# Kernel optimization log

Measured on AMD Instinct MI355X. Metric: run time of the kernel, lower is better.

Reference implementation:

```python
import jax, jax.numpy as jnp
import numpy as np

B, S, D = 64, 512, 1024  # batch, seq_len, units (input_dim == units required by module)
UNITS = D


def setup_inputs() -> dict:
    key = jax.random.key(0)
    k1, k2, k3 = jax.random.split(key, 3)
    inputs = jax.random.normal(k1, (B, S, D), dtype=jnp.float32)
    # kernel / recurrent_kernel: (input_dim, 4*units), gate column order [i, f, c, o]
    scale = 1.0 / np.sqrt(D)
    W = jax.random.normal(k2, (D, 4 * UNITS), dtype=jnp.float32) * scale
    U = jax.random.normal(k3, (D, 4 * UNITS), dtype=jnp.float32) * scale
    b = jnp.zeros((4 * UNITS,), dtype=jnp.float32)
    return {"inputs": inputs, "W": W, "U": U, "b": b}


def _lstm(inputs, W, U, b):
    units = W.shape[1] // 4
    h0 = jnp.zeros((inputs.shape[0], units), dtype=inputs.dtype)
    c0 = jnp.zeros((inputs.shape[0], units), dtype=inputs.dtype)
    # Precompute input projections for all timesteps in one big GEMM: [B,S,4U]
    x_proj = jnp.einsum("bsd,dg->bsg", inputs, W) + b
    x_proj_t = jnp.swapaxes(x_proj, 0, 1)  # [S,B,4U] time-major

    def step(carry, xp):
        ht, ct = carry
        z = xp + ht @ U  # [B,4U]
        i = jax.nn.sigmoid(z[:, :units])
        f = jax.nn.sigmoid(z[:, units:2 * units])
        c_t = jnp.tanh(z[:, 2 * units:3 * units])
        o = jax.nn.sigmoid(z[:, 3 * units:])
        ct = f * ct + i * c_t
        ht = o * jnp.tanh(ct)
        return (ht, ct), ht

    (ht, ct), outs = jax.lax.scan(step, (h0, c0), x_proj_t)
    outputs = jnp.swapaxes(outs, 0, 1)  # [B,S,U]
    return outputs, ht, ct


def reference(inputs, W, U, b):
    return _lstm(inputs, W, U, b)
```

## Files before the change

### kernel.cpp

```cpp
#include <hip/hip_runtime.h>
#include <hip/hip_bf16.h>
#include <cstdint>
#include <cstddef>

#define BB 64
#define SS 512
#define DD 1024
#define G4 4096

typedef __attribute__((ext_vector_type(8))) short bf16x8;
typedef __attribute__((ext_vector_type(8))) unsigned short u16x8;
typedef __attribute__((ext_vector_type(4))) float f32x4;

static __device__ __forceinline__ unsigned short f2bf(float f) {
  union { float f; uint32_t u; } v; v.f = f;
  uint32_t u = v.u;
  return (unsigned short)((u + 0x7FFFu + ((u >> 16) & 1u)) >> 16);
}
static __device__ __forceinline__ float bf2f(unsigned short s) {
  union { uint32_t u; float f; } v; v.u = ((uint32_t)s) << 16; return v.f;
}

typedef __attribute__((address_space(1))) const unsigned int kGlbU32;
typedef __attribute__((address_space(3))) unsigned int kLdsU32;
static __device__ __forceinline__ void gload_lds16(const void* g, void* l) {
  __builtin_amdgcn_global_load_lds((kGlbU32*)g, (kLdsU32*)l, 16, 0, 0);
}

__global__ void cvt_x(const float* __restrict__ in, unsigned short* __restrict__ out, int n8) {
  for (int i = blockIdx.x * blockDim.x + threadIdx.x; i < n8; i += gridDim.x * blockDim.x) {
    const float4* pp = (const float4*)(in + (size_t)i * 8);
    float4 a = pp[0], b2 = pp[1];
    u16x8 o;
    o[0] = f2bf(a.x);  o[1] = f2bf(a.y);  o[2] = f2bf(a.z);  o[3] = f2bf(a.w);
    o[4] = f2bf(b2.x); o[5] = f2bf(b2.y); o[6] = f2bf(b2.z); o[7] = f2bf(b2.w);
    *(u16x8*)(out + (size_t)i * 8) = o;
  }
}

__global__ __launch_bounds__(256) void cvt_transpose(
    const float* __restrict__ Win, const float* __restrict__ Uin,
    unsigned short* __restrict__ Wt, unsigned short* __restrict__ Ut) {
  __shared__ float tile[32][33];
  const float* in = blockIdx.z ? Uin : Win;
  unsigned short* out = blockIdx.z ? Ut : Wt;
  int k0 = blockIdx.x * 32;
  int c0 = blockIdx.y * 32;
  int tc = threadIdx.x & 31, tr = threadIdx.x >> 5;
  #pragma unroll
  for (int j = 0; j < 32; j += 8)
    tile[tr + j][tc] = in[(size_t)(k0 + tr + j) * G4 + (c0 + tc)];
  __syncthreads();
  #pragma unroll
  for (int j = 0; j < 32; j += 8)
    out[(size_t)(c0 + tr + j) * DD + (k0 + tc)] = f2bf(tile[tc][tr + j]);
}

__global__ __launch_bounds__(256) void pack_u(const unsigned short* __restrict__ Ut,
                                              unsigned short* __restrict__ Up) {
  int tid = blockIdx.x * 256 + threadIdx.x;
  int l = tid & 63;
  int kk = (tid >> 6) & 31;
  int g = (tid >> 11) & 3;
  int u = tid >> 13;
  int col = g * DD + u * 16 + (l & 15);
  int k = kk * 32 + (l >> 4) * 8;
  bf16x8 v = *(const bf16x8*)(Ut + (size_t)col * DD + k);
  *(bf16x8*)(Up + (size_t)tid * 8) = v;
}

__global__ __launch_bounds__(256) void gemm_xproj(
    const unsigned short* __restrict__ xb,
    const unsigned short* __restrict__ Wt,
    const float* __restrict__ bias,
    unsigned short* __restrict__ xproj) {
  __shared__ unsigned short As[128 * 64], Bs[128 * 64];
  const int tid = threadIdx.x;
  const int wave = tid >> 6, lane = tid & 63;
  const int wr = wave >> 1, wc = wave & 1;
  const int m0 = blockIdx.x * 128, n0 = blockIdx.y * 128;

  const int srow = tid >> 1, shalf = tid & 1;
  const unsigned short* ga = xb + (size_t)(m0 + srow) * DD + shalf * 32;
  const unsigned short* gb = Wt + (size_t)(n0 + srow) * DD + shalf * 32;

  bf16x8 ra[4], rb[4];
  #pragma unroll
  for (int c = 0; c < 4; ++c) {
    ra[c] = *(const bf16x8*)(ga + c * 8);
    rb[c] = *(const bf16x8*)(gb + c * 8);
  }

  f32x4 acc[4][4];
  #pragma unroll
  for (int m = 0; m < 4; ++m)
    #pragma unroll
    for (int n = 0; n < 4; ++n) acc[m][n] = (f32x4){0.f, 0.f, 0.f, 0.f};

  char* asb = (char*)As;
  char* bsb = (char*)Bs;

  for (int kt = 0; kt < DD / 64; ++kt) {
    __syncthreads();
    #pragma unroll
    for (int c = 0; c < 4; ++c) {
      int wb = srow * 128 + ((shalf * 64 + c * 16) ^ ((srow & 7) << 4));
      *(bf16x8*)(asb + wb) = ra[c];
      *(bf16x8*)(bsb + wb) = rb[c];
    }
    __syncthreads();
    if (kt + 1 < DD / 64) {
      #pragma unroll
      for (int c = 0; c < 4; ++c) {
        ra[c] = *(const bf16x8*)(ga + (kt + 1) * 64 + c * 8);
        rb[c] = *(const bf16x8*)(gb + (kt + 1) * 64 + c * 8);
      }
    }
    #pragma unroll
    for (int kh = 0; kh < 2; ++kh) {
      bf16x8 af[4], bfr[4];
      const int kb = kh * 64 + (lane >> 4) * 16;
      #pragma unroll
      for (int m = 0; m < 4; ++m) {
        int row = wr * 64 + m * 16 + (lane & 15);
        af[m] = *(const bf16x8*)(asb + row * 128 + (kb ^ ((row & 7) << 4)));
        int coln = wc * 64 + m * 16 + (lane & 15);
        bfr[m] = *(const bf16x8*)(bsb + coln * 128 + (kb ^ ((coln & 7) << 4)));
      }
      #pragma unroll
      for (int m = 0; m < 4; ++m)
        #pragma unroll
        for (int n = 0; n < 4; ++n)
          acc[m][n] = __builtin_amdgcn_mfma_f32_16x16x32_bf16(af[m], bfr[n], acc[m][n], 0, 0, 0);
    }
  }

  #pragma unroll
  for (int n = 0; n < 4; ++n) {
    int col = n0 + wc * 64 + n * 16 + (lane & 15);
    int g = col >> 10, unit = col & 1023;
    int ugrp2 = unit >> 4, uc2 = unit & 15;
    float bv = bias[col];
    #pragma unroll
    for (int m = 0; m < 4; ++m) {
      #pragma unroll
      for (int j = 0; j < 4; ++j) {
        int mrow = m0 + wr * 64 + m * 16 + (lane >> 4) * 4 + j;
        int b = mrow >> 9, t2 = mrow & 511;
        size_t idx = ((((size_t)t2 * 4 + (b >> 4)) * 64 + ugrp2) * 256 + (b & 15) * 16 + uc2) * 4 + g;
        xproj[idx] = f2bf(acc[m][n][j] + bv);
      }
    }
  }
}

__global__ __launch_bounds__(256, 1) void lstm_persist(
    const unsigned short* __restrict__ xproj,
    const unsigned short* __restrict__ Up,
    unsigned short* __restrict__ h0,
    unsigned short* __restrict__ h1,
    unsigned int* __restrict__ bar,
    float* __restrict__ out) {
  extern __shared__ char smem[];
  const int bid = blockIdx.x;
  const int rgrp = (bid & 7) >> 1;
  const int ugrp = (bid >> 3) * 2 + (bid & 1);
  const int tid = threadIdx.x;
  const int wave = tid >> 6, lane = tid & 63;
  const int r = tid >> 4, uc = tid & 15;
  const int row = rgrp * 16 + r, unit = ugrp * 16 + uc;

  char* upw = smem + wave * 30720;
  float (*zt)[16][16] = (float (*)[16][16])(smem + 122880);

  const char* ug = (const char*)Up + (size_t)(ugrp * 4 + wave) * 32768;
  #pragma unroll
  for (int kk = 0; kk < 30; ++kk)
    gload_lds16(ug + kk * 1024 + lane * 16, upw + kk * 1024 + lane * 16);
  bf16x8 u30 = *(const bf16x8*)(ug + 30 * 1024 + lane * 16);
  bf16x8 u31 = *(const bf16x8*)(ug + 31 * 1024 + lane * 16);

  const unsigned short* xp = xproj + (((size_t)rgrp * 64 + ugrp) * 256 + tid) * 4;
  const int hnidx = ((rgrp * 32 + (unit >> 5)) * 64 + ((unit >> 3) & 3) * 16 + r) * 8 + (unit & 7);
  unsigned int* myflags = bar + rgrp * 64;
  float c = 0.f;
  ushort4 xv = *(const ushort4*)xp;

  asm volatile("s_waitcnt vmcnt(0)" ::: "memory");
  __builtin_amdgcn_sched_barrier(0);
  __syncthreads();

  const bf16x8* uv = (const bf16x8*)upw;
  f32x4 z4 = {0.f, 0.f, 0.f, 0.f};
  unsigned fv = 0;

  for (int t = 0; t < SS; ++t) {
    #pragma unroll
    for (int j = 0; j < 4; ++j)
      zt[wave][(lane >> 4) * 4 + j][lane & 15] = z4[j];
    __syncthreads();

    float zi = zt[0][r][uc] + bf2f(xv.x);
    float zf = zt[1][r][uc] + bf2f(xv.y);
    float zg = zt[2][r][uc] + bf2f(xv.z);
    float zo = zt[3][r][uc] + bf2f(xv.w);
    float ig = 1.f / (1.f + __expf(-zi));
    float fg = 1.f / (1.f + __expf(-zf));
    float gg = 1.f - 2.f / (1.f + __expf(2.f * zg));
    float og = 1.f / (1.f + __expf(-zo));
    c = fg * c + ig * gg;
    float h = og * (1.f - 2.f / (1.f + __expf(2.f * c)));

    if (t == SS - 1) {
      out[((size_t)row * SS + t) * DD + unit] = h;
      const size_t S0 = (size_t)BB * SS * DD;
      out[S0 + (size_t)row * DD + unit] = h;
      out[S0 + (size_t)BB * DD + (size_t)row * DD + unit] = c;
      break;
    }

    unsigned short* hn = (t & 1) ? h0 : h1;
    __hip_atomic_store(hn + hnidx, f2bf(h), __ATOMIC_RELAXED, __HIP_MEMORY_SCOPE_AGENT);
    __syncthreads();
    if (tid == 0)
      __hip_atomic_store(myflags + ugrp, (unsigned)(t + 1), __ATOMIC_RELAXED, __HIP_MEMORY_SCOPE_AGENT);
    out[((size_t)row * SS + t) * DD + unit] = h;
    xv = *(const ushort4*)(xp + (size_t)(t + 1) * 262144);

    const char* hb = (const char*)((t & 1) ? h0 : h1) + rgrp * 32768 + lane * 16;
    const unsigned tgt = (unsigned)(t + 1);
    f32x4 a0 = {0.f,0.f,0.f,0.f}, a1 = a0, a2 = a0, a3 = a0;
    #pragma unroll
    for (int b = 0; b < 4; ++b) {
      while ((( __ballot((int)(fv >= tgt)) >> (16 * b)) & 0xFFFFull) != 0xFFFFull)
        fv = __hip_atomic_load(myflags + lane, __ATOMIC_RELAXED, __HIP_MEMORY_SCOPE_AGENT);
      bf16x8 av0, av1, av2, av3, av4, av5, av6, av7;
      const char* hbb = hb + b * 8192;
      asm volatile("global_load_dwordx4 %0, %1, off sc0 sc1" : "=v"(av0) : "v"(hbb + 0 * 1024) : "memory");
      asm volatile("global_load_dwordx4 %0, %1, off sc0 sc1" : "=v"(av1) : "v"(hbb + 1 * 1024) : "memory");
      asm volatile("global_load_dwordx4 %0, %1, off sc0 sc1" : "=v"(av2) : "v"(hbb + 2 * 1024) : "memory");
      asm volatile("global_load_dwordx4 %0, %1, off sc0 sc1" : "=v"(av3) : "v"(hbb + 3 * 1024) : "memory");
      asm volatile("global_load_dwordx4 %0, %1, off sc0 sc1" : "=v"(av4) : "v"(hbb + 4 * 1024) : "memory");
      asm volatile("global_load_dwordx4 %0, %1, off sc0 sc1" : "=v"(av5) : "v"(hbb + 5 * 1024) : "memory");
      asm volatile("global_load_dwordx4 %0, %1, off sc0 sc1" : "=v"(av6) : "v"(hbb + 6 * 1024) : "memory");
      asm volatile("global_load_dwordx4 %0, %1, off sc0 sc1" : "=v"(av7) : "v"(hbb + 7 * 1024) : "memory");
      asm volatile("s_waitcnt vmcnt(0)" ::: "memory");
      __builtin_amdgcn_sched_barrier(0);
      const int k0 = b * 8;
      a0 = __builtin_amdgcn_mfma_f32_16x16x32_bf16(av0, (k0 + 0 < 30) ? uv[(k0 + 0) * 64 + lane] : ((k0 + 0 == 30) ? u30 : u31), a0, 0, 0, 0);
      a1 = __builtin_amdgcn_mfma_f32_16x16x32_bf16(av1, (k0 + 1 < 30) ? uv[(k0 + 1) * 64 + lane] : ((k0 + 1 == 30) ? u30 : u31), a1, 0, 0, 0);
      a2 = __builtin_amdgcn_mfma_f32_16x16x32_bf16(av2, (k0 + 2 < 30) ? uv[(k0 + 2) * 64 + lane] : ((k0 + 2 == 30) ? u30 : u31), a2, 0, 0, 0);
      a3 = __builtin_amdgcn_mfma_f32_16x16x32_bf16(av3, (k0 + 3 < 30) ? uv[(k0 + 3) * 64 + lane] : ((k0 + 3 == 30) ? u30 : u31), a3, 0, 0, 0);
      a0 = __builtin_amdgcn_mfma_f32_16x16x32_bf16(av4, (k0 + 4 < 30) ? uv[(k0 + 4) * 64 + lane] : ((k0 + 4 == 30) ? u30 : u31), a0, 0, 0, 0);
      a1 = __builtin_amdgcn_mfma_f32_16x16x32_bf16(av5, (k0 + 5 < 30) ? uv[(k0 + 5) * 64 + lane] : ((k0 + 5 == 30) ? u30 : u31), a1, 0, 0, 0);
      a2 = __builtin_amdgcn_mfma_f32_16x16x32_bf16(av6, (k0 + 6 < 30) ? uv[(k0 + 6) * 64 + lane] : ((k0 + 6 == 30) ? u30 : u31), a2, 0, 0, 0);
      a3 = __builtin_amdgcn_mfma_f32_16x16x32_bf16(av7, (k0 + 7 < 30) ? uv[(k0 + 7) * 64 + lane] : ((k0 + 7 == 30) ? u30 : u31), a3, 0, 0, 0);
    }
    z4 = (a0 + a1) + (a2 + a3);
  }
}

template <bool XBF>
__global__ __launch_bounds__(256) void lstm_step(
    const unsigned short* __restrict__ xb, const float* __restrict__ xf,
    const unsigned short* __restrict__ Wt, const unsigned short* __restrict__ Ut,
    const float* __restrict__ bias, unsigned short* __restrict__ hbuf,
    float* __restrict__ cbuf, float* __restrict__ out, int t) {
  __shared__ float ztl[4][16][16];
  const int wg = blockIdx.x;
  const int ugrp = wg >> 2, rgrp = wg & 3;
  const int row0 = rgrp * 16;
  const int ucol0 = ugrp * 16;
  const int wave = threadIdx.x >> 6;
  const int lane = threadIdx.x & 63;
  const int k0 = (lane >> 4) * 8;
  const int gr = row0 + (lane & 15);
  const int cg = wave * DD + ucol0 + (lane & 15);

  const unsigned short* hp = hbuf + (size_t)(t & 1) * BB * DD + (size_t)gr * DD + k0;
  const unsigned short* wp = Wt + (size_t)cg * DD + k0;
  const unsigned short* up = Ut + (size_t)cg * DD + k0;

  f32x4 acc = {0.f, 0.f, 0.f, 0.f};
  if (XBF) {
    const unsigned short* xpp = xb + ((size_t)gr * SS + t) * DD + k0;
    #pragma unroll 8
    for (int kk = 0; kk < DD; kk += 32) {
      bf16x8 a = *(const bf16x8*)(xpp + kk);
      bf16x8 b = *(const bf16x8*)(wp + kk);
      acc = __builtin_amdgcn_mfma_f32_16x16x32_bf16(a, b, acc, 0, 0, 0);
    }
  } else {
    const float* xpp = xf + ((size_t)gr * SS + t) * DD + k0;
    #pragma unroll 4
    for (int kk = 0; kk < DD; kk += 32) {
      float4 v0 = *(const float4*)(xpp + kk);
      float4 v1 = *(const float4*)(xpp + kk + 4);
      bf16x8 a;
      a[0] = (short)f2bf(v0.x); a[1] = (short)f2bf(v0.y);
      a[2] = (short)f2bf(v0.z); a[3] = (short)f2bf(v0.w);
      a[4] = (short)f2bf(v1.x); a[5] = (short)f2bf(v1.y);
      a[6] = (short)f2bf(v1.z); a[7] = (short)f2bf(v1.w);
      bf16x8 b = *(const bf16x8*)(wp + kk);
      acc = __builtin_amdgcn_mfma_f32_16x16x32_bf16(a, b, acc, 0, 0, 0);
    }
  }
  #pragma unroll 8
  for (int kk = 0; kk < DD; kk += 32) {
    bf16x8 a = *(const bf16x8*)(hp + kk);
    bf16x8 b = *(const bf16x8*)(up + kk);
    acc = __builtin_amdgcn_mfma_f32_16x16x32_bf16(a, b, acc, 0, 0, 0);
  }

  float bv = bias[cg];
  #pragma unroll
  for (int j = 0; j < 4; ++j)
    ztl[wave][(lane >> 4) * 4 + j][lane & 15] = acc[j] + bv;
  __syncthreads();

  const int r = threadIdx.x >> 4, uc = threadIdx.x & 15;
  float zi = ztl[0][r][uc], zf = ztl[1][r][uc], zg = ztl[2][r][uc], zo = ztl[3][r][uc];
  float ig = 1.f / (1.f + __expf(-zi));
  float fg = 1.f / (1.f + __expf(-zf));
  float gg = tanhf(zg);
  float og = 1.f / (1.f + __expf(-zo));
  const int gidx = (row0 + r) * DD + ucol0 + uc;
  float c = fg * cbuf[gidx] + ig * gg;
  cbuf[gidx] = c;
  float h = og * tanhf(c);
  hbuf[(size_t)((t & 1) ^ 1) * BB * DD + gidx] = f2bf(h);
  out[((size_t)(row0 + r) * SS + t) * DD + ucol0 + uc] = h;
  if (t == SS - 1) {
    out[(size_t)BB * SS * DD + gidx] = h;
    out[(size_t)BB * SS * DD + BB * DD + gidx] = c;
  }
}

extern "C" void kernel_launch(void* const* d_in, const int* in_sizes, int n_in,
                              void* d_out, int out_size, void* d_ws, size_t ws_size,
                              hipStream_t stream) {
  const float* x = (const float*)d_in[0];
  const float* W = (const float*)d_in[1];
  const float* U = (const float*)d_in[2];
  const float* bias = (const float*)d_in[3];
  float* out = (float*)d_out;
  char* ws = (char*)d_ws;

  const size_t oWt = 0;
  const size_t oUt = oWt + (size_t)G4 * DD * 2;
  const size_t oH0 = oUt + (size_t)G4 * DD * 2;
  const size_t oH1 = oH0 + (size_t)BB * DD * 2;
  const size_t oC  = oH1 + (size_t)BB * DD * 2;
  const size_t oBar = oC + (size_t)BB * DD * 4;
  const size_t oXb = oBar + 4096;
  const size_t oUp = oXb + (size_t)BB * SS * DD * 2;
  const size_t oXp = oUp + (size_t)G4 * DD * 2;
  const size_t needPersist = oXp + (size_t)SS * BB * G4 * 2;
  const size_t needR1x = oUp;

  unsigned short* Wt = (unsigned short*)(ws + oWt);
  unsigned short* Ut = (unsigned short*)(ws + oUt);
  unsigned short* h0 = (unsigned short*)(ws + oH0);
  unsigned short* h1 = (unsigned short*)(ws + oH1);
  float* cbuf = (float*)(ws + oC);
  unsigned int* bar = (unsigned int*)(ws + oBar);
  unsigned short* xb = (unsigned short*)(ws + oXb);
  unsigned short* Up = (unsigned short*)(ws + oUp);
  unsigned short* xproj = (unsigned short*)(ws + oXp);

  if (ws_size >= needPersist) {
    hipFuncSetAttribute((const void*)lstm_persist,
                        hipFuncAttributeMaxDynamicSharedMemorySize, 126976);
    hipMemsetAsync(h0, 0, (size_t)BB * DD * 2, stream);
    hipMemsetAsync(bar, 0, 4096, stream);
    cvt_transpose<<<dim3(32, 128, 2), 256, 0, stream>>>(W, U, Wt, Ut);
    pack_u<<<2048, 256, 0, stream>>>(Ut, Up);
    cvt_x<<<2048, 256, 0, stream>>>(x, xb, BB * SS * DD / 8);
    gemm_xproj<<<dim3(256, 32), 256, 0, stream>>>(xb, Wt, bias, xproj);
    lstm_persist<<<256, 256, 126976, stream>>>(xproj, Up, h0, h1, bar, out);
  } else {
    unsigned short* hbuf = h0;
    const bool xbf = ws_size >= needR1x;
    hipMemsetAsync(hbuf, 0, (size_t)2 * BB * DD * 2 + (size_t)BB * DD * 4, stream);
    cvt_transpose<<<dim3(32, 128, 2), 256, 0, stream>>>(W, U, Wt, Ut);
    if (xbf) cvt_x<<<2048, 256, 0, stream>>>(x, xb, BB * SS * DD / 8);
    for (int t = 0; t < SS; ++t) {
      if (xbf)
        lstm_step<true><<<256, 256, 0, stream>>>(xb, nullptr, Wt, Ut, bias, hbuf, cbuf, out, t);
      else
        lstm_step<false><<<256, 256, 0, stream>>>(nullptr, x, Wt, Ut, bias, hbuf, cbuf, out, t);
    }
  }
}
```

Before: 2.462 ms.

## Wait on all flags once, then load full hidden state via atomic loads

Replaces the staged per-quarter flag polling plus inline-asm sc0/sc1 loads with one wait on all 64 producer flags, followed by 64 relaxed 64-bit atomic loads of the whole hidden vector. It also remaps the thread-to-(row,unit) assignment so each thread's h store goes to a contiguous offset (hoff = ... + tid). The intent is to drop the repeated ballot/poll rounds and issue all h loads back to back before the MFMA chain. In exchange, loading can no longer overlap with producers that finish late, register pressure rises from 64 live 64-bit values, and coherence now depends on atomic-load semantics instead of explicit cache-bypass flags.

```diff
diff --git a/kernel.cpp b/kernel.cpp
--- a/kernel.cpp
+++ b/kernel.cpp
@@ -167,8 +167,10 @@
   const int ugrp = (bid >> 3) * 2 + (bid & 1);
   const int tid = threadIdx.x;
   const int wave = tid >> 6, lane = tid & 63;
-  const int r = tid >> 4, uc = tid & 15;
-  const int row = rgrp * 16 + r, unit = ugrp * 16 + uc;
+  const int row = (tid >> 3) & 15;
+  const int uc = (tid >> 7) * 8 + (tid & 7);
+  const int unit = ugrp * 16 + uc;
+  const int grow = rgrp * 16 + row;
 
   char* upw = smem + wave * 30720;
   float (*zt)[16][16] = (float (*)[16][16])(smem + 122880);
@@ -180,8 +182,8 @@
   bf16x8 u30 = *(const bf16x8*)(ug + 30 * 1024 + lane * 16);
   bf16x8 u31 = *(const bf16x8*)(ug + 31 * 1024 + lane * 16);
 
-  const unsigned short* xp = xproj + (((size_t)rgrp * 64 + ugrp) * 256 + tid) * 4;
-  const int hnidx = ((rgrp * 32 + (unit >> 5)) * 64 + ((unit >> 3) & 3) * 16 + r) * 8 + (unit & 7);
+  const unsigned short* xp = xproj + (((size_t)rgrp * 64 + ugrp) * 256 + row * 16 + uc) * 4;
+  const size_t hoff = (size_t)rgrp * 16384 + (size_t)(ugrp >> 1) * 512 + (size_t)(ugrp & 1) * 256 + tid;
   unsigned int* myflags = bar + rgrp * 64;
   float c = 0.f;
   ushort4 xv = *(const ushort4*)xp;
@@ -200,10 +202,10 @@
       zt[wave][(lane >> 4) * 4 + j][lane & 15] = z4[j];
     __syncthreads();
 
-    float zi = zt[0][r][uc] + bf2f(xv.x);
-    float zf = zt[1][r][uc] + bf2f(xv.y);
-    float zg = zt[2][r][uc] + bf2f(xv.z);
-    float zo = zt[3][r][uc] + bf2f(xv.w);
+    float zi = zt[0][row][uc] + bf2f(xv.x);
+    float zf = zt[1][row][uc] + bf2f(xv.y);
+    float zg = zt[2][row][uc] + bf2f(xv.z);
+    float zo = zt[3][row][uc] + bf2f(xv.w);
     float ig = 1.f / (1.f + __expf(-zi));
     float fg = 1.f / (1.f + __expf(-zf));
     float gg = 1.f - 2.f / (1.f + __expf(2.f * zg));
@@ -212,49 +214,50 @@
     float h = og * (1.f - 2.f / (1.f + __expf(2.f * c)));
 
     if (t == SS - 1) {
-      out[((size_t)row * SS + t) * DD + unit] = h;
+      out[((size_t)grow * SS + t) * DD + unit] = h;
       const size_t S0 = (size_t)BB * SS * DD;
-      out[S0 + (size_t)row * DD + unit] = h;
-      out[S0 + (size_t)BB * DD + (size_t)row * DD + unit] = c;
+      out[S0 + (size_t)grow * DD + unit] = h;
+      out[S0 + (size_t)BB * DD + (size_t)grow * DD + unit] = c;
       break;
     }
 
     unsigned short* hn = (t & 1) ? h0 : h1;
-    __hip_atomic_store(hn + hnidx, f2bf(h), __ATOMIC_RELAXED, __HIP_MEMORY_SCOPE_AGENT);
+    __hip_atomic_store(hn + hoff, f2bf(h), __ATOMIC_RELAXED, __HIP_MEMORY_SCOPE_AGENT);
     __syncthreads();
     if (tid == 0)
       __hip_atomic_store(myflags + ugrp, (unsigned)(t + 1), __ATOMIC_RELAXED, __HIP_MEMORY_SCOPE_AGENT);
-    out[((size_t)row * SS + t) * DD + unit] = h;
+    out[((size_t)grow * SS + t) * DD + unit] = h;
     xv = *(const ushort4*)(xp + (size_t)(t + 1) * 262144);
 
-    const char* hb = (const char*)((t & 1) ? h0 : h1) + rgrp * 32768 + lane * 16;
     const unsigned tgt = (unsigned)(t + 1);
+    while (!__all((int)(fv >= tgt)))
+      fv = __hip_atomic_load(myflags + lane, __ATOMIC_RELAXED, __HIP_MEMORY_SCOPE_AGENT);
+
+    const unsigned long long* hq =
+        (const unsigned long long*)((t & 1) ? h0 : h1) + (size_t)rgrp * 4096 + lane * 2;
+    unsigned long long lo[32], hi[32];
+    #pragma unroll
+    for (int i = 0; i < 32; ++i) {
+      lo[i] = __hip_atomic_load(hq + (size_t)i * 128,     __ATOMIC_RELAXED, __HIP_MEMORY_SCOPE_AGENT);
+      hi[i] = __hip_atomic_load(hq + (size_t)i * 128 + 1, __ATOMIC_RELAXED, __HIP_MEMORY_SCOPE_AGENT);
+    }
+
     f32x4 a0 = {0.f,0.f,0.f,0.f}, a1 = a0, a2 = a0, a3 = a0;
     #pragma unroll
-    for (int b = 0; b < 4; ++b) {
-      while ((( __ballot((int)(fv >= tgt)) >> (16 * b)) & 0xFFFFull) != 0xFFFFull)
-        fv = __hip_atomic_load(myflags + lane, __ATOMIC_RELAXED, __HIP_MEMORY_SCOPE_AGENT);
-      bf16x8 av0, av1, av2, av3, av4, av5, av6, av7;
-      const char* hbb = hb + b * 8192;
-      asm volatile("global_load_dwordx4 %0, %1, off sc0 sc1" : "=v"(av0) : "v"(hbb + 0 * 1024) : "memory");
-      asm volatile("global_load_dwordx4 %0, %1, off sc0 sc1" : "=v"(av1) : "v"(hbb + 1 * 1024) : "memory");
-      asm volatile("global_load_dwordx4 %0, %1, off sc0 sc1" : "=v"(av2) : "v"(hbb + 2 * 1024) : "memory");
-      asm volatile("global_load_dwordx4 %0, %1, off sc0 sc1" : "=v"(av3) : "v"(hbb + 3 * 1024) : "memory");
-      asm volatile("global_load_dwordx4 %0, %1, off sc0 sc1" : "=v"(av4) : "v"(hbb + 4 * 1024) : "memory");
-      asm volatile("global_load_dwordx4 %0, %1, off sc0 sc1" : "=v"(av5) : "v"(hbb + 5 * 1024) : "memory");
-      asm volatile("global_load_dwordx4 %0, %1, off sc0 sc1" : "=v"(av6) : "v"(hbb + 6 * 1024) : "memory");
-      asm volatile("global_load_dwordx4 %0, %1, off sc0 sc1" : "=v"(av7) : "v"(hbb + 7 * 1024) : "memory");
-      asm volatile("s_waitcnt vmcnt(0)" ::: "memory");
-      __builtin_amdgcn_sched_barrier(0);
-      const int k0 = b * 8;
-      a0 = __builtin_amdgcn_mfma_f32_16x16x32_bf16(av0, (k0 + 0 < 30) ? uv[(k0 + 0) * 64 + lane] : ((k0 + 0 == 30) ? u30 : u31), a0, 0, 0, 0);
-      a1 = __builtin_amdgcn_mfma_f32_16x16x32_bf16(av1, (k0 + 1 < 30) ? uv[(k0 + 1) * 64 + lane] : ((k0 + 1 == 30) ? u30 : u31), a1, 0, 0, 0);
-      a2 = __builtin_amdgcn_mfma_f32_16x16x32_bf16(av2, (k0 + 2 < 30) ? uv[(k0 + 2) * 64 + lane] : ((k0 + 2 == 30) ? u30 : u31), a2, 0, 0, 0);
-      a3 = __builtin_amdgcn_mfma_f32_16x16x32_bf16(av3, (k0 + 3 < 30) ? uv[(k0 + 3) * 64 + lane] : ((k0 + 3 == 30) ? u30 : u31), a3, 0, 0, 0);
-      a0 = __builtin_amdgcn_mfma_f32_16x16x32_bf16(av4, (k0 + 4 < 30) ? uv[(k0 + 4) * 64 + lane] : ((k0 + 4 == 30) ? u30 : u31), a0, 0, 0, 0);
-      a1 = __builtin_amdgcn_mfma_f32_16x16x32_bf16(av5, (k0 + 5 < 30) ? uv[(k0 + 5) * 64 + lane] : ((k0 + 5 == 30) ? u30 : u31), a1, 0, 0, 0);
-      a2 = __builtin_amdgcn_mfma_f32_16x16x32_bf16(av6, (k0 + 6 < 30) ? uv[(k0 + 6) * 64 + lane] : ((k0 + 6 == 30) ? u30 : u31), a2, 0, 0, 0);
-      a3 = __builtin_amdgcn_mfma_f32_16x16x32_bf16(av7, (k0 + 7 < 30) ? uv[(k0 + 7) * 64 + lane] : ((k0 + 7 == 30) ? u30 : u31), a3, 0, 0, 0);
+    for (int i = 0; i < 32; i += 4) {
+      union { unsigned long long q[2]; bf16x8 v; } w0, w1, w2, w3;
+      w0.q[0] = lo[i + 0]; w0.q[1] = hi[i + 0];
+      w1.q[0] = lo[i + 1]; w1.q[1] = hi[i + 1];
+      w2.q[0] = lo[i + 2]; w2.q[1] = hi[i + 2];
+      w3.q[0] = lo[i + 3]; w3.q[1] = hi[i + 3];
+      bf16x8 b0 = (i + 0 < 30) ? uv[(i + 0) * 64 + lane] : ((i + 0 == 30) ? u30 : u31);
+      bf16x8 b1 = (i + 1 < 30) ? uv[(i + 1) * 64 + lane] : ((i + 1 == 30) ? u30 : u31);
+      bf16x8 b2 = (i + 2 < 30) ? uv[(i + 2) * 64 + lane] : ((i + 2 == 30) ? u30 : u31);
+      bf16x8 b3 = (i + 3 < 30) ? uv[(i + 3) * 64 + lane] : ((i + 3 == 30) ? u30 : u31);
+      a0 = __builtin_amdgcn_mfma_f32_16x16x32_bf16(w0.v, b0, a0, 0, 0, 0);
+      a1 = __builtin_amdgcn_mfma_f32_16x16x32_bf16(w1.v, b1, a1, 0, 0, 0);
+      a2 = __builtin_amdgcn_mfma_f32_16x16x32_bf16(w2.v, b2, a2, 0, 0, 0);
+      a3 = __builtin_amdgcn_mfma_f32_16x16x32_bf16(w3.v, b3, a3, 0, 0, 0);
     }
     z4 = (a0 + a1) + (a2 + a3);
   }
```

New measurement: 2.667 ms. +8.3%, slower.

## Fuse input projection GEMM into persistent LSTM kernel per timestep

Applied to the files above, without the earlier changes.

Removes the separate x·W GEMM and its large bf16 xproj buffer. Each timestep, the persistent kernel now stages the next x rows into LDS and computes its x·W slice with MFMA, reading packed W from global/L2, while other blocks finish the hidden state. This is meant to save the big GEMM pass and the xproj write and read, and to hide the projection work under the barrier wait. In exchange it adds W reads and MFMA work on every step of the serial critical path, and needs more LDS.

```diff
diff --git a/kernel.cpp b/kernel.cpp
--- a/kernel.cpp
+++ b/kernel.cpp
@@ -69,97 +69,14 @@
   *(bf16x8*)(Up + (size_t)tid * 8) = v;
 }
 
-__global__ __launch_bounds__(256) void gemm_xproj(
+__global__ __launch_bounds__(256, 1) void lstm_persist(
     const unsigned short* __restrict__ xb,
-    const unsigned short* __restrict__ Wt,
-    const float* __restrict__ bias,
-    unsigned short* __restrict__ xproj) {
-  __shared__ unsigned short As[128 * 64], Bs[128 * 64];
-  const int tid = threadIdx.x;
-  const int wave = tid >> 6, lane = tid & 63;
-  const int wr = wave >> 1, wc = wave & 1;
-  const int m0 = blockIdx.x * 128, n0 = blockIdx.y * 128;
-
-  const int srow = tid >> 1, shalf = tid & 1;
-  const unsigned short* ga = xb + (size_t)(m0 + srow) * DD + shalf * 32;
-  const unsigned short* gb = Wt + (size_t)(n0 + srow) * DD + shalf * 32;
-
-  bf16x8 ra[4], rb[4];
-  #pragma unroll
-  for (int c = 0; c < 4; ++c) {
-    ra[c] = *(const bf16x8*)(ga + c * 8);
-    rb[c] = *(const bf16x8*)(gb + c * 8);
-  }
-
-  f32x4 acc[4][4];
-  #pragma unroll
-  for (int m = 0; m < 4; ++m)
-    #pragma unroll
-    for (int n = 0; n < 4; ++n) acc[m][n] = (f32x4){0.f, 0.f, 0.f, 0.f};
-
-  char* asb = (char*)As;
-  char* bsb = (char*)Bs;
-
-  for (int kt = 0; kt < DD / 64; ++kt) {
-    __syncthreads();
-    #pragma unroll
-    for (int c = 0; c < 4; ++c) {
-      int wb = srow * 128 + ((shalf * 64 + c * 16) ^ ((srow & 7) << 4));
-      *(bf16x8*)(asb + wb) = ra[c];
-      *(bf16x8*)(bsb + wb) = rb[c];
-    }
-    __syncthreads();
-    if (kt + 1 < DD / 64) {
-      #pragma unroll
-      for (int c = 0; c < 4; ++c) {
-        ra[c] = *(const bf16x8*)(ga + (kt + 1) * 64 + c * 8);
-        rb[c] = *(const bf16x8*)(gb + (kt + 1) * 64 + c * 8);
-      }
-    }
-    #pragma unroll
-    for (int kh = 0; kh < 2; ++kh) {
-      bf16x8 af[4], bfr[4];
-      const int kb = kh * 64 + (lane >> 4) * 16;
-      #pragma unroll
-      for (int m = 0; m < 4; ++m) {
-        int row = wr * 64 + m * 16 + (lane & 15);
-        af[m] = *(const bf16x8*)(asb + row * 128 + (kb ^ ((row & 7) << 4)));
-        int coln = wc * 64 + m * 16 + (lane & 15);
-        bfr[m] = *(const bf16x8*)(bsb + coln * 128 + (kb ^ ((coln & 7) << 4)));
-      }
-      #pragma unroll
-      for (int m = 0; m < 4; ++m)
-        #pragma unroll
-        for (int n = 0; n < 4; ++n)
-          acc[m][n] = __builtin_amdgcn_mfma_f32_16x16x32_bf16(af[m], bfr[n], acc[m][n], 0, 0, 0);
-    }
-  }
-
-  #pragma unroll
-  for (int n = 0; n < 4; ++n) {
-    int col = n0 + wc * 64 + n * 16 + (lane & 15);
-    int g = col >> 10, unit = col & 1023;
-    int ugrp2 = unit >> 4, uc2 = unit & 15;
-    float bv = bias[col];
-    #pragma unroll
-    for (int m = 0; m < 4; ++m) {
-      #pragma unroll
-      for (int j = 0; j < 4; ++j) {
-        int mrow = m0 + wr * 64 + m * 16 + (lane >> 4) * 4 + j;
-        int b = mrow >> 9, t2 = mrow & 511;
-        size_t idx = ((((size_t)t2 * 4 + (b >> 4)) * 64 + ugrp2) * 256 + (b & 15) * 16 + uc2) * 4 + g;
-        xproj[idx] = f2bf(acc[m][n][j] + bv);
-      }
-    }
-  }
-}
-
-__global__ __launch_bounds__(256, 1) void lstm_persist(
-    const unsigned short* __restrict__ xproj,
     const unsigned short* __restrict__ Up,
+    const unsigned short* __restrict__ Wp,
     unsigned short* __restrict__ h0,
     unsigned short* __restrict__ h1,
     unsigned int* __restrict__ bar,
+    const float* __restrict__ bias,
     float* __restrict__ out) {
   extern __shared__ char smem[];
   const int bid = blockIdx.x;
@@ -167,11 +84,14 @@
   const int ugrp = (bid >> 3) * 2 + (bid & 1);
   const int tid = threadIdx.x;
   const int wave = tid >> 6, lane = tid & 63;
-  const int r = tid >> 4, uc = tid & 15;
-  const int row = rgrp * 16 + r, unit = ugrp * 16 + uc;
+  const int row = (tid >> 3) & 15;
+  const int uc = (tid >> 7) * 8 + (tid & 7);
+  const int unit = ugrp * 16 + uc;
+  const int grow = rgrp * 16 + row;
 
   char* upw = smem + wave * 30720;
-  float (*zt)[16][16] = (float (*)[16][16])(smem + 122880);
+  char* xs  = smem + 122880;
+  float (*zt)[16][16] = (float (*)[16][16])(smem + 155648);
 
   const char* ug = (const char*)Up + (size_t)(ugrp * 4 + wave) * 32768;
   #pragma unroll
@@ -179,31 +99,77 @@
     gload_lds16(ug + kk * 1024 + lane * 16, upw + kk * 1024 + lane * 16);
   bf16x8 u30 = *(const bf16x8*)(ug + 30 * 1024 + lane * 16);
   bf16x8 u31 = *(const bf16x8*)(ug + 31 * 1024 + lane * 16);
-
-  const unsigned short* xp = xproj + (((size_t)rgrp * 64 + ugrp) * 256 + tid) * 4;
-  const int hnidx = ((rgrp * 32 + (unit >> 5)) * 64 + ((unit >> 3) & 3) * 16 + r) * 8 + (unit & 7);
+  const char* wgb = (const char*)Wp + (size_t)(ugrp * 4 + wave) * 32768;
+
+  const float bi0 = bias[unit], bi1 = bias[DD + unit],
+              bi2 = bias[2 * DD + unit], bi3 = bias[3 * DD + unit];
+
+  const size_t hoff = (size_t)rgrp * 16384 + (size_t)(ugrp >> 1) * 512 +
+                      (size_t)(ugrp & 1) * 256 + tid;
   unsigned int* myflags = bar + rgrp * 64;
   float c = 0.f;
-  ushort4 xv = *(const ushort4*)xp;
-
+
+#define STAGE_X(TT)                                                            \
+  {                                                                            \
+    _Pragma("unroll")                                                          \
+    for (int i = 0; i < 8; ++i) {                                              \
+      const int ch = wave * 8 + i;                                             \
+      const int xrow = ch >> 1;                                                \
+      const int kbyte = (ch & 1) * 1024 + lane * 16;                           \
+      const int ksw = kbyte ^ ((xrow & 7) << 4);                               \
+      const char* src = (const char*)xb +                                      \
+          ((size_t)(rgrp * 16 + xrow) * SS + (TT)) * 2048 + ksw;               \
+      gload_lds16(src, xs + ch * 1024 + lane * 16);                            \
+    }                                                                          \
+  }
+
+#define XW_COMPUTE(ZXOUT)                                                      \
+  {                                                                            \
+    f32x4 x0 = {0.f, 0.f, 0.f, 0.f}, x1 = x0, x2 = x0, x3 = x0;                \
+    _Pragma("unroll")                                                          \
+    for (int half = 0; half < 2; ++half) {                                     \
+      bf16x8 wv[16];                                                           \
+      _Pragma("unroll")                                                        \
+      for (int i = 0; i < 16; ++i)                                             \
+        wv[i] = *(const bf16x8*)(wgb + (half * 16 + i) * 1024 + lane * 16);    \
+      _Pragma("unroll")                                                        \
+      for (int i = 0; i < 16; i += 4) {                                        \
+        const int kk = half * 16 + i;                                          \
+        const int arow = (lane & 15) * 2048;                                   \
+        const int swz = (lane & 7) << 4;                                       \
+        bf16x8 af0 = *(const bf16x8*)(xs + arow + (((kk + 0) * 64 + (lane >> 4) * 16) ^ swz)); \
+        bf16x8 af1 = *(const bf16x8*)(xs + arow + (((kk + 1) * 64 + (lane >> 4) * 16) ^ swz)); \
+        bf16x8 af2 = *(const bf16x8*)(xs + arow + (((kk + 2) * 64 + (lane >> 4) * 16) ^ swz)); \
+        bf16x8 af3 = *(const bf16x8*)(xs + arow + (((kk + 3) * 64 + (lane >> 4) * 16) ^ swz)); \
+        x0 = __builtin_amdgcn_mfma_f32_16x16x32_bf16(af0, wv[i + 0], x0, 0, 0, 0); \
+        x1 = __builtin_amdgcn_mfma_f32_16x16x32_bf16(af1, wv[i + 1], x1, 0, 0, 0); \
+        x2 = __builtin_amdgcn_mfma_f32_16x16x32_bf16(af2, wv[i + 2], x2, 0, 0, 0); \
+        x3 = __builtin_amdgcn_mfma_f32_16x16x32_bf16(af3, wv[i + 3], x3, 0, 0, 0); \
+      }                                                                        \
+    }                                                                          \
+    ZXOUT = (x0 + x1) + (x2 + x3);                                             \
+  }
+
+  STAGE_X(0);
   asm volatile("s_waitcnt vmcnt(0)" ::: "memory");
   __builtin_amdgcn_sched_barrier(0);
   __syncthreads();
 
-  const bf16x8* uv = (const bf16x8*)upw;
+  f32x4 zx4;
+  XW_COMPUTE(zx4);
   f32x4 z4 = {0.f, 0.f, 0.f, 0.f};
   unsigned fv = 0;
 
   for (int t = 0; t < SS; ++t) {
     #pragma unroll
     for (int j = 0; j < 4; ++j)
-      zt[wave][(lane >> 4) * 4 + j][lane & 15] = z4[j];
+      zt[wave][(lane >> 4) * 4 + j][lane & 15] = z4[j] + zx4[j];
     __syncthreads();
 
-    float zi = zt[0][r][uc] + bf2f(xv.x);
-    float zf = zt[1][r][uc] + bf2f(xv.y);
-    float zg = zt[2][r][uc] + bf2f(xv.z);
-    float zo = zt[3][r][uc] + bf2f(xv.w);
+    float zi = zt[0][row][uc] + bi0;
+    float zf = zt[1][row][uc] + bi1;
+    float zg = zt[2][row][uc] + bi2;
+    float zo = zt[3][row][uc] + bi3;
     float ig = 1.f / (1.f + __expf(-zi));
     float fg = 1.f / (1.f + __expf(-zf));
     float gg = 1.f - 2.f / (1.f + __expf(2.f * zg));
@@ -212,27 +178,33 @@
     float h = og * (1.f - 2.f / (1.f + __expf(2.f * c)));
 
     if (t == SS - 1) {
-      out[((size_t)row * SS + t) * DD + unit] = h;
+      out[((size_t)grow * SS + t) * DD + unit] = h;
       const size_t S0 = (size_t)BB * SS * DD;
-      out[S0 + (size_t)row * DD + unit] = h;
-      out[S0 + (size_t)BB * DD + (size_t)row * DD + unit] = c;
+      out[S0 + (size_t)grow * DD + unit] = h;
+      out[S0 + (size_t)BB * DD + (size_t)grow * DD + unit] = c;
       break;
     }
 
+    STAGE_X(t + 1);
+
     unsigned short* hn = (t & 1) ? h0 : h1;
-    __hip_atomic_store(hn + hnidx, f2bf(h), __ATOMIC_RELAXED, __HIP_MEMORY_SCOPE_AGENT);
+    __hip_atomic_store(hn + hoff, f2bf(h), __ATOMIC_RELAXED, __HIP_MEMORY_SCOPE_AGENT);
     __syncthreads();
     if (tid == 0)
       __hip_atomic_store(myflags + ugrp, (unsigned)(t + 1), __ATOMIC_RELAXED, __HIP_MEMORY_SCOPE_AGENT);
-    out[((size_t)row * SS + t) * DD + unit] = h;
-    xv = *(const ushort4*)(xp + (size_t)(t + 1) * 262144);
-
-    const char* hb = (const char*)((t & 1) ? h0 : h1) + rgrp * 32768 + lane * 16;
+    out[((size_t)grow * SS + t) * DD + unit] = h;
+    XW_COMPUTE(zx4);
+
+    asm volatile("s_waitcnt vmcnt(0)" ::: "memory");
+    __builtin_amdgcn_sched_barrier(0);
+
     const unsigned tgt = (unsigned)(t + 1);
+    const char* hb = (const char*)((t & 1) ? h0 : h1) + (size_t)rgrp * 32768 + lane * 16;
+    const bf16x8* uv = (const bf16x8*)upw;
     f32x4 a0 = {0.f,0.f,0.f,0.f}, a1 = a0, a2 = a0, a3 = a0;
     #pragma unroll
     for (int b = 0; b < 4; ++b) {
-      while ((( __ballot((int)(fv >= tgt)) >> (16 * b)) & 0xFFFFull) != 0xFFFFull)
+      while (((__ballot((int)(fv >= tgt)) >> (16 * b)) & 0xFFFFull) != 0xFFFFull)
         fv = __hip_atomic_load(myflags + lane, __ATOMIC_RELAXED, __HIP_MEMORY_SCOPE_AGENT);
       bf16x8 av0, av1, av2, av3, av4, av5, av6, av7;
       const char* hbb = hb + b * 8192;
@@ -258,6 +230,8 @@
     }
     z4 = (a0 + a1) + (a2 + a3);
   }
+#undef STAGE_X
+#undef XW_COMPUTE
 }
 
 template <bool XBF>
@@ -354,8 +328,8 @@
   const size_t oBar = oC + (size_t)BB * DD * 4;
   const size_t oXb = oBar + 4096;
   const size_t oUp = oXb + (size_t)BB * SS * DD * 2;
-  const size_t oXp = oUp + (size_t)G4 * DD * 2;
-  const size_t needPersist = oXp + (size_t)SS * BB * G4 * 2;
+  const size_t oWp = oUp + (size_t)G4 * DD * 2;
+  const size_t needFused = oWp + (size_t)G4 * DD * 2;
   const size_t needR1x = oUp;
 
   unsigned short* Wt = (unsigned short*)(ws + oWt);
@@ -366,18 +340,18 @@
   unsigned int* bar = (unsigned int*)(ws + oBar);
   unsigned short* xb = (unsigned short*)(ws + oXb);
   unsigned short* Up = (unsigned short*)(ws + oUp);
-  unsigned short* xproj = (unsigned short*)(ws + oXp);
-
-  if (ws_size >= needPersist) {
+  unsigned short* Wp = (unsigned short*)(ws + oWp);
+
+  if (ws_size >= needFused) {
     hipFuncSetAttribute((const void*)lstm_persist,
-                        hipFuncAttributeMaxDynamicSharedMemorySize, 126976);
+                        hipFuncAttributeMaxDynamicSharedMemorySize, 159744);
     hipMemsetAsync(h0, 0, (size_t)BB * DD * 2, stream);
     hipMemsetAsync(bar, 0, 4096, stream);
     cvt_transpose<<<dim3(32, 128, 2), 256, 0, stream>>>(W, U, Wt, Ut);
     pack_u<<<2048, 256, 0, stream>>>(Ut, Up);
+    pack_u<<<2048, 256, 0, stream>>>(Wt, Wp);
     cvt_x<<<2048, 256, 0, stream>>>(x, xb, BB * SS * DD / 8);
-    gemm_xproj<<<dim3(256, 32), 256, 0, stream>>>(xb, Wt, bias, xproj);
-    lstm_persist<<<256, 256, 126976, stream>>>(xproj, Up, h0, h1, bar, out);
+    lstm_persist<<<256, 256, 159744, stream>>>(xb, Up, Wp, h0, h1, bar, bias, out);
   } else {
     unsigned short* hbuf = h0;
     const bool xbf = ws_size >= needR1x;
```

Result: slower. 2.711 ms (+10.1%).

## Load GEMM tiles directly to LDS and store xproj gate-planar

Applied to the files above, without the earlier changes.

The input-projection GEMM now copies tiles global-to-LDS with direct load instructions and a pre-swizzled source offset, replacing the register-staged prefetch. The prefetch overlap is dropped: the kernel waits for the loads before each compute step. The xproj output layout also changes from gate-interleaved (4 adjacent bf16 per element) to four separate gate planes. The GEMM epilogue stores become contiguous 2-byte writes across lanes instead of stride-8-byte scatter. The recurrent kernel now issues four scalar loads per step instead of one 8-byte vector load.

```diff
diff --git a/kernel.cpp b/kernel.cpp
--- a/kernel.cpp
+++ b/kernel.cpp
@@ -80,42 +80,32 @@
   const int wr = wave >> 1, wc = wave & 1;
   const int m0 = blockIdx.x * 128, n0 = blockIdx.y * 128;
 
-  const int srow = tid >> 1, shalf = tid & 1;
-  const unsigned short* ga = xb + (size_t)(m0 + srow) * DD + shalf * 32;
-  const unsigned short* gb = Wt + (size_t)(n0 + srow) * DD + shalf * 32;
-
-  bf16x8 ra[4], rb[4];
-  #pragma unroll
-  for (int c = 0; c < 4; ++c) {
-    ra[c] = *(const bf16x8*)(ga + c * 8);
-    rb[c] = *(const bf16x8*)(gb + c * 8);
-  }
-
-  f32x4 acc[4][4];
-  #pragma unroll
-  for (int m = 0; m < 4; ++m)
-    #pragma unroll
-    for (int n = 0; n < 4; ++n) acc[m][n] = (f32x4){0.f, 0.f, 0.f, 0.f};
-
   char* asb = (char*)As;
   char* bsb = (char*)Bs;
 
+  const int srw = lane >> 3;
+  const int skb = (((lane & 7) ^ srw) << 4);
+
+  f32x4 acc[4][4];
+  #pragma unroll
+  for (int m = 0; m < 4; ++m)
+    #pragma unroll
+    for (int n = 0; n < 4; ++n) acc[m][n] = (f32x4){0.f, 0.f, 0.f, 0.f};
+
   for (int kt = 0; kt < DD / 64; ++kt) {
     __syncthreads();
     #pragma unroll
-    for (int c = 0; c < 4; ++c) {
-      int wb = srow * 128 + ((shalf * 64 + c * 16) ^ ((srow & 7) << 4));
-      *(bf16x8*)(asb + wb) = ra[c];
-      *(bf16x8*)(bsb + wb) = rb[c];
-    }
+    for (int q = 0; q < 4; ++q) {
+      const int c = wave * 4 + q;
+      gload_lds16((const char*)xb + (size_t)(m0 + c * 8 + srw) * 2048 + kt * 128 + skb,
+                  asb + c * 1024 + lane * 16);
+      gload_lds16((const char*)Wt + (size_t)(n0 + c * 8 + srw) * 2048 + kt * 128 + skb,
+                  bsb + c * 1024 + lane * 16);
+    }
+    asm volatile("s_waitcnt vmcnt(0)" ::: "memory");
+    __builtin_amdgcn_sched_barrier(0);
     __syncthreads();
-    if (kt + 1 < DD / 64) {
-      #pragma unroll
-      for (int c = 0; c < 4; ++c) {
-        ra[c] = *(const bf16x8*)(ga + (kt + 1) * 64 + c * 8);
-        rb[c] = *(const bf16x8*)(gb + (kt + 1) * 64 + c * 8);
-      }
-    }
+
     #pragma unroll
     for (int kh = 0; kh < 2; ++kh) {
       bf16x8 af[4], bfr[4];
@@ -147,7 +137,8 @@
       for (int j = 0; j < 4; ++j) {
         int mrow = m0 + wr * 64 + m * 16 + (lane >> 4) * 4 + j;
         int b = mrow >> 9, t2 = mrow & 511;
-        size_t idx = ((((size_t)t2 * 4 + (b >> 4)) * 64 + ugrp2) * 256 + (b & 15) * 16 + uc2) * 4 + g;
+        size_t idx = ((((size_t)g * SS + t2) * 4 + (b >> 4)) * 64 + ugrp2) * 256
+                     + (b & 15) * 16 + uc2;
         xproj[idx] = f2bf(acc[m][n][j] + bv);
       }
     }
@@ -180,11 +171,12 @@
   bf16x8 u30 = *(const bf16x8*)(ug + 30 * 1024 + lane * 16);
   bf16x8 u31 = *(const bf16x8*)(ug + 31 * 1024 + lane * 16);
 
-  const unsigned short* xp = xproj + (((size_t)rgrp * 64 + ugrp) * 256 + tid) * 4;
+  const size_t GSTRIDE = (size_t)SS * 4 * 64 * 256;
+  const unsigned short* xp = xproj + (((size_t)rgrp * 64 + ugrp) * 256 + tid);
   const int hnidx = ((rgrp * 32 + (unit >> 5)) * 64 + ((unit >> 3) & 3) * 16 + r) * 8 + (unit & 7);
   unsigned int* myflags = bar + rgrp * 64;
   float c = 0.f;
-  ushort4 xv = *(const ushort4*)xp;
+  unsigned short xv0 = xp[0], xv1 = xp[GSTRIDE], xv2 = xp[2 * GSTRIDE], xv3 = xp[3 * GSTRIDE];
 
   asm volatile("s_waitcnt vmcnt(0)" ::: "memory");
   __builtin_amdgcn_sched_barrier(0);
@@ -200,10 +192,10 @@
       zt[wave][(lane >> 4) * 4 + j][lane & 15] = z4[j];
     __syncthreads();
 
-    float zi = zt[0][r][uc] + bf2f(xv.x);
-    float zf = zt[1][r][uc] + bf2f(xv.y);
-    float zg = zt[2][r][uc] + bf2f(xv.z);
-    float zo = zt[3][r][uc] + bf2f(xv.w);
+    float zi = zt[0][r][uc] + bf2f(xv0);
+    float zf = zt[1][r][uc] + bf2f(xv1);
+    float zg = zt[2][r][uc] + bf2f(xv2);
+    float zo = zt[3][r][uc] + bf2f(xv3);
     float ig = 1.f / (1.f + __expf(-zi));
     float fg = 1.f / (1.f + __expf(-zf));
     float gg = 1.f - 2.f / (1.f + __expf(2.f * zg));
@@ -225,7 +217,13 @@
     if (tid == 0)
       __hip_atomic_store(myflags + ugrp, (unsigned)(t + 1), __ATOMIC_RELAXED, __HIP_MEMORY_SCOPE_AGENT);
     out[((size_t)row * SS + t) * DD + unit] = h;
-    xv = *(const ushort4*)(xp + (size_t)(t + 1) * 262144);
+    {
+      const size_t o = (size_t)(t + 1) * 65536;
+      xv0 = xp[o];
+      xv1 = xp[GSTRIDE + o];
+      xv2 = xp[2 * GSTRIDE + o];
+      xv3 = xp[3 * GSTRIDE + o];
+    }
 
     const char* hb = (const char*)((t & 1) ? h0 : h1) + rgrp * 32768 + lane * 16;
     const unsigned tgt = (unsigned)(t + 1);
```

After: 2.325 ms. -5.6%, faster.
